# Kernel tuning notes

Measured on AMD Instinct MI355X. Metric: run time of the kernel, lower is better.

The kernel has to match this reference:

```python
import jax, jax.numpy as jnp
import numpy as np

INPUT_SIZE = 84 * 84 * 4  # 28224
FEATURE_SIZE = 1500
BATCH = 256

def setup_inputs() -> dict:
    key = jax.random.key(0)
    k_x, k_we, k_wd = jax.random.split(key, 3)
    scale_e = 1.0 / np.sqrt(INPUT_SIZE)
    scale_d = 1.0 / np.sqrt(FEATURE_SIZE)
    return {
        "x": jax.random.normal(k_x, (BATCH, INPUT_SIZE), dtype=jnp.float32),
        "W_enc": jax.random.normal(k_we, (FEATURE_SIZE, INPUT_SIZE), dtype=jnp.float32) * scale_e,
        "b_enc": jnp.zeros((FEATURE_SIZE,), dtype=jnp.float32),
        "W_dec": jax.random.normal(k_wd, (INPUT_SIZE, FEATURE_SIZE), dtype=jnp.float32) * scale_d,
        "b_dec": jnp.zeros((INPUT_SIZE,), dtype=jnp.float32),
    }

def reference(x, W_enc, b_enc, W_dec, b_dec):
    # Encoder: y_enc = sigmoid(x @ W_enc^T + b_enc), shape [B, F]
    y_enc = jax.nn.sigmoid(jnp.einsum('bi,fi->bf', x, W_enc) + b_enc)
    # Contractive (Jacobian Frobenius norm) term, closed form:
    # d y_enc[b,i] / d x[b,:] = y*(1-y) * W_enc[i,:]
    # jac_reg = sum_{b,i} (y*(1-y))^2 * ||W_enc[i,:]||^2
    s2 = jnp.square(y_enc * (1.0 - y_enc))          # [B, F]
    row_norm2 = jnp.sum(jnp.square(W_enc), axis=1)  # [F]
    jac_reg = jnp.sum(s2 * row_norm2)               # scalar
    # Decoder
    y_out = jax.nn.sigmoid(jnp.einsum('bf,if->bi', y_enc, W_dec) + b_dec)
    return y_out, jac_reg
```

## Files before the change

### kernel.cpp

```cpp
#include <hip/hip_runtime.h>
#include <hip/hip_bf16.h>


#define BATCH 256
#define IN    28224
#define FEAT  1500

typedef __attribute__((ext_vector_type(8))) short short8;
typedef __attribute__((ext_vector_type(4))) float f32x4;

__device__ __forceinline__ unsigned short f2bf(float f) {
    unsigned int u = __float_as_uint(f);
    u = (u + 0x7FFFu + ((u >> 16) & 1u)) >> 16;
    return (unsigned short)u;
}

#define ENC_KCH 1344

__global__ __launch_bounds__(256) void enc_gemm(const float* __restrict__ x,
                                                const float* __restrict__ We,
                                                float* __restrict__ preact,
                                                float* __restrict__ rn2) {
    const int n0 = blockIdx.x * 64;
    const int kbase = blockIdx.y * ENC_KCH;

    __shared__ unsigned short As[256 * 40];
    __shared__ unsigned short Bs[64 * 40];
    __shared__ float rowsq[64];

    const int t    = threadIdx.x;
    const int lane = t & 63;
    const int w    = t >> 6;
    const int l15  = lane & 15;
    const int quad = lane >> 4;

    if (t < 64) rowsq[t] = 0.0f;
    __syncthreads();

    f32x4 acc[4][4];
#pragma unroll
    for (int mt = 0; mt < 4; ++mt)
#pragma unroll
        for (int nt = 0; nt < 4; ++nt) { f32x4 z = {0.f, 0.f, 0.f, 0.f}; acc[mt][nt] = z; }

    for (int kt = 0; kt < ENC_KCH / 32; ++kt) {
        const int k0 = kbase + kt * 32;
#pragma unroll
        for (int j = 0; j < 8; ++j) {
            int idx = t + 256 * j;
            int row = idx >> 3;
            int c4  = idx & 7;
            const float4 v = *(const float4*)(x + row * IN + k0 + c4 * 4);
            ushort4 h;
            h.x = f2bf(v.x); h.y = f2bf(v.y); h.z = f2bf(v.z); h.w = f2bf(v.w);
            *(ushort4*)&As[row * 40 + c4 * 4] = h;
        }
#pragma unroll
        for (int j = 0; j < 2; ++j) {
            int idx = t + 256 * j;
            int row = idx >> 3;
            int c4  = idx & 7;
            int f   = n0 + row;
            float4 v = make_float4(0.f, 0.f, 0.f, 0.f);
            if (f < FEAT) v = *(const float4*)(We + (long)f * IN + k0 + c4 * 4);
            ushort4 h;
            h.x = f2bf(v.x); h.y = f2bf(v.y); h.z = f2bf(v.z); h.w = f2bf(v.w);
            *(ushort4*)&Bs[row * 40 + c4 * 4] = h;
            float sq = v.x * v.x + v.y * v.y + v.z * v.z + v.w * v.w;
            atomicAdd(&rowsq[row], sq);
        }
        __syncthreads();

        short8 a[4], b[4];
#pragma unroll
        for (int mt = 0; mt < 4; ++mt)
            a[mt] = *(const short8*)&As[(w * 64 + mt * 16 + l15) * 40 + quad * 8];
#pragma unroll
        for (int nt = 0; nt < 4; ++nt)
            b[nt] = *(const short8*)&Bs[(nt * 16 + l15) * 40 + quad * 8];
#pragma unroll
        for (int mt = 0; mt < 4; ++mt)
#pragma unroll
            for (int nt = 0; nt < 4; ++nt)
                acc[mt][nt] = __builtin_amdgcn_mfma_f32_16x16x32_bf16(a[mt], b[nt], acc[mt][nt], 0, 0, 0);
        __syncthreads();
    }

#pragma unroll
    for (int mt = 0; mt < 4; ++mt) {
#pragma unroll
        for (int nt = 0; nt < 4; ++nt) {
            int col = n0 + nt * 16 + l15;
            if (col < FEAT) {
#pragma unroll
                for (int r = 0; r < 4; ++r) {
                    int row = w * 64 + mt * 16 + quad * 4 + r;
                    atomicAdd(&preact[row * FEAT + col], acc[mt][nt][r]);
                }
            }
        }
    }

    if (t < 64) {
        int f = n0 + t;
        if (f < FEAT) atomicAdd(&rn2[f], rowsq[t]);
    }
}

__global__ __launch_bounds__(256) void act_jac(const float* __restrict__ preact,
                                               const float* __restrict__ be,
                                               const float* __restrict__ rn2,
                                               unsigned short* __restrict__ yenc,
                                               float* __restrict__ jac) {
    const int b = blockIdx.y;
    const int f = blockIdx.x * 256 + threadIdx.x;
    float local = 0.0f;
    unsigned short h = 0;
    if (f < FEAT) {
        float p = preact[b * FEAT + f] + be[f];
        float y = 1.0f / (1.0f + __expf(-p));
        h = f2bf(y);
        float s = y * (1.0f - y);
        local = s * s * rn2[f];
    }
    yenc[b * 1536 + f] = h;

    float v = local;
#pragma unroll
    for (int off = 32; off > 0; off >>= 1) v += __shfl_down(v, off);
    __shared__ float red[4];
    const int lane = threadIdx.x & 63;
    const int w = threadIdx.x >> 6;
    if (lane == 0) red[w] = v;
    __syncthreads();
    if (threadIdx.x == 0) atomicAdd(jac, red[0] + red[1] + red[2] + red[3]);
}

__global__ __launch_bounds__(256) void dec_gemm(const unsigned short* __restrict__ yenc,
                                                const float* __restrict__ Wd,
                                                const float* __restrict__ bd,
                                                float* __restrict__ out) {
    const int n0 = blockIdx.x * 64;

    __shared__ unsigned short As[256 * 40];
    __shared__ unsigned short Bs[64 * 40];

    const int t    = threadIdx.x;
    const int lane = t & 63;
    const int w    = t >> 6;
    const int l15  = lane & 15;
    const int quad = lane >> 4;

    f32x4 acc[4][4];
#pragma unroll
    for (int mt = 0; mt < 4; ++mt)
#pragma unroll
        for (int nt = 0; nt < 4; ++nt) { f32x4 z = {0.f, 0.f, 0.f, 0.f}; acc[mt][nt] = z; }

    for (int kt = 0; kt < 48; ++kt) {
        const int k0 = kt * 32;
#pragma unroll
        for (int j = 0; j < 4; ++j) {
            int idx = t + 256 * j;
            int row = idx >> 2;
            int c   = idx & 3;
            const short8 v = *(const short8*)(yenc + row * 1536 + k0 + c * 8);
            *(short8*)&As[row * 40 + c * 8] = v;
        }
#pragma unroll
        for (int j = 0; j < 2; ++j) {
            int idx = t + 256 * j;
            int row = idx >> 3;
            int c4  = idx & 7;
            int i   = n0 + row;
            int k   = k0 + c4 * 4;
            float4 v = make_float4(0.f, 0.f, 0.f, 0.f);
            if (k < 1500) v = *(const float4*)(Wd + (long)i * FEAT + k);
            ushort4 h;
            h.x = f2bf(v.x); h.y = f2bf(v.y); h.z = f2bf(v.z); h.w = f2bf(v.w);
            *(ushort4*)&Bs[row * 40 + c4 * 4] = h;
        }
        __syncthreads();

        short8 a[4], b[4];
#pragma unroll
        for (int mt = 0; mt < 4; ++mt)
            a[mt] = *(const short8*)&As[(w * 64 + mt * 16 + l15) * 40 + quad * 8];
#pragma unroll
        for (int nt = 0; nt < 4; ++nt)
            b[nt] = *(const short8*)&Bs[(nt * 16 + l15) * 40 + quad * 8];
#pragma unroll
        for (int mt = 0; mt < 4; ++mt)
#pragma unroll
            for (int nt = 0; nt < 4; ++nt)
                acc[mt][nt] = __builtin_amdgcn_mfma_f32_16x16x32_bf16(a[mt], b[nt], acc[mt][nt], 0, 0, 0);
        __syncthreads();
    }

#pragma unroll
    for (int mt = 0; mt < 4; ++mt) {
#pragma unroll
        for (int nt = 0; nt < 4; ++nt) {
            int col = n0 + nt * 16 + l15;
            float bias = bd[col];
#pragma unroll
            for (int r = 0; r < 4; ++r) {
                int row = w * 64 + mt * 16 + quad * 4 + r;
                float v = acc[mt][nt][r] + bias;
                out[row * IN + col] = 1.0f / (1.0f + __expf(-v));
            }
        }
    }
}

extern "C" void kernel_launch(void* const* d_in, const int* in_sizes, int n_in,
                              void* d_out, int out_size, void* d_ws, size_t ws_size,
                              hipStream_t stream) {
    const float* x  = (const float*)d_in[0];
    const float* We = (const float*)d_in[1];
    const float* be = (const float*)d_in[2];
    const float* Wd = (const float*)d_in[3];
    const float* bd = (const float*)d_in[4];
    float* out = (float*)d_out;

    char* ws = (char*)d_ws;
    float* preact          = (float*)ws;
    float* rn2             = (float*)(ws + 1536000);
    unsigned short* yenc   = (unsigned short*)(ws + 1544192);

    hipMemsetAsync(ws, 0, 1544192, stream);
    hipMemsetAsync(out + 7225344, 0, 4, stream);

    enc_gemm<<<dim3(24, 21), 256, 0, stream>>>(x, We, preact, rn2);
    act_jac<<<dim3(6, 256), 256, 0, stream>>>(preact, be, rn2, yenc, out + 7225344);
    dec_gemm<<<dim3(441, 1), 256, 0, stream>>>(yenc, Wd, bd, out);
}
```

Measured before the change: 576.1 us.

## Pre-convert x to bf16 and load MFMA operands directly from global memory

A separate kernel converts x to bf16 once into workspace. Both GEMMs then drop LDS staging and barriers, with each lane loading its MFMA fragments straight from global memory and converting weights using a cheaper perm-based bf16 pack. The encoder split-K is doubled to 42 chunks, and row norms are accumulated in registers with shuffles instead of shared-memory atomics. Costs include an extra pass over x, more preact atomics, round-half-up instead of round-to-even conversion, and strided uncoalesced global loads with no cross-wave reuse through LDS.

```diff
diff --git a/kernel.cpp b/kernel.cpp
--- a/kernel.cpp
+++ b/kernel.cpp
@@ -5,105 +5,112 @@
 #define BATCH 256
 #define IN    28224
 #define FEAT  1500
+#define FPAD  1536
 
 typedef __attribute__((ext_vector_type(8))) short short8;
 typedef __attribute__((ext_vector_type(4))) float f32x4;
 
-__device__ __forceinline__ unsigned short f2bf(float f) {
-    unsigned int u = __float_as_uint(f);
-    u = (u + 0x7FFFu + ((u >> 16) & 1u)) >> 16;
-    return (unsigned short)u;
-}
-
-#define ENC_KCH 1344
-
-__global__ __launch_bounds__(256) void enc_gemm(const float* __restrict__ x,
+__device__ __forceinline__ unsigned pack2(float lo, float hi) {
+    unsigned a = __float_as_uint(lo) + 0x8000u;
+    unsigned b = __float_as_uint(hi) + 0x8000u;
+    return __builtin_amdgcn_perm(b, a, 0x07060302);
+}
+
+__device__ __forceinline__ short8 cvt8(const float4 v0, const float4 v1) {
+    union { short8 s; unsigned u[4]; } r;
+    r.u[0] = pack2(v0.x, v0.y);
+    r.u[1] = pack2(v0.z, v0.w);
+    r.u[2] = pack2(v1.x, v1.y);
+    r.u[3] = pack2(v1.z, v1.w);
+    return r.s;
+}
+
+__global__ __launch_bounds__(256) void cvt_x(const float* __restrict__ x,
+                                             unsigned short* __restrict__ xbf) {
+    int idx = blockIdx.x * 256 + threadIdx.x;
+    float4 v = ((const float4*)x)[idx];
+    ((uint2*)xbf)[idx] = make_uint2(pack2(v.x, v.y), pack2(v.z, v.w));
+}
+
+__global__ __launch_bounds__(256) void enc_gemm(const unsigned short* __restrict__ xbf,
                                                 const float* __restrict__ We,
                                                 float* __restrict__ preact,
                                                 float* __restrict__ rn2) {
-    const int n0 = blockIdx.x * 64;
-    const int kbase = blockIdx.y * ENC_KCH;
-
-    __shared__ unsigned short As[256 * 40];
-    __shared__ unsigned short Bs[64 * 40];
-    __shared__ float rowsq[64];
-
+    const int n0   = blockIdx.x * 64;
+    const int kb   = blockIdx.y * 672;
     const int t    = threadIdx.x;
     const int lane = t & 63;
     const int w    = t >> 6;
     const int l15  = lane & 15;
     const int quad = lane >> 4;
-
-    if (t < 64) rowsq[t] = 0.0f;
-    __syncthreads();
+    const int m0   = w * 64;
+
+    const unsigned short* ap[4];
+#pragma unroll
+    for (int mt = 0; mt < 4; ++mt)
+        ap[mt] = xbf + (long)(m0 + mt * 16 + l15) * IN + quad * 8 + kb;
+
+    const float* bp[4];
+    int fcol[4];
+#pragma unroll
+    for (int nt = 0; nt < 4; ++nt) {
+        int f = n0 + nt * 16 + l15;
+        fcol[nt] = f;
+        int fc = f < FEAT ? f : FEAT - 1;
+        bp[nt] = We + (long)fc * IN + quad * 8 + kb;
+    }
 
     f32x4 acc[4][4];
 #pragma unroll
     for (int mt = 0; mt < 4; ++mt)
 #pragma unroll
         for (int nt = 0; nt < 4; ++nt) { f32x4 z = {0.f, 0.f, 0.f, 0.f}; acc[mt][nt] = z; }
-
-    for (int kt = 0; kt < ENC_KCH / 32; ++kt) {
-        const int k0 = kbase + kt * 32;
-#pragma unroll
-        for (int j = 0; j < 8; ++j) {
-            int idx = t + 256 * j;
-            int row = idx >> 3;
-            int c4  = idx & 7;
-            const float4 v = *(const float4*)(x + row * IN + k0 + c4 * 4);
-            ushort4 h;
-            h.x = f2bf(v.x); h.y = f2bf(v.y); h.z = f2bf(v.z); h.w = f2bf(v.w);
-            *(ushort4*)&As[row * 40 + c4 * 4] = h;
-        }
-#pragma unroll
-        for (int j = 0; j < 2; ++j) {
-            int idx = t + 256 * j;
-            int row = idx >> 3;
-            int c4  = idx & 7;
-            int f   = n0 + row;
-            float4 v = make_float4(0.f, 0.f, 0.f, 0.f);
-            if (f < FEAT) v = *(const float4*)(We + (long)f * IN + k0 + c4 * 4);
-            ushort4 h;
-            h.x = f2bf(v.x); h.y = f2bf(v.y); h.z = f2bf(v.z); h.w = f2bf(v.w);
-            *(ushort4*)&Bs[row * 40 + c4 * 4] = h;
-            float sq = v.x * v.x + v.y * v.y + v.z * v.z + v.w * v.w;
-            atomicAdd(&rowsq[row], sq);
-        }
-        __syncthreads();
-
-        short8 a[4], b[4];
-#pragma unroll
-        for (int mt = 0; mt < 4; ++mt)
-            a[mt] = *(const short8*)&As[(w * 64 + mt * 16 + l15) * 40 + quad * 8];
-#pragma unroll
-        for (int nt = 0; nt < 4; ++nt)
-            b[nt] = *(const short8*)&Bs[(nt * 16 + l15) * 40 + quad * 8];
+    float rsq[4] = {0.f, 0.f, 0.f, 0.f};
+
+    for (int k = 0; k < 672; k += 32) {
+        short8 a[4];
+#pragma unroll
+        for (int mt = 0; mt < 4; ++mt)
+            a[mt] = *(const short8*)(ap[mt] + k);
+        short8 bb[4];
+#pragma unroll
+        for (int nt = 0; nt < 4; ++nt) {
+            const float4 b0 = *(const float4*)(bp[nt] + k);
+            const float4 b1 = *(const float4*)(bp[nt] + k + 4);
+            bb[nt] = cvt8(b0, b1);
+            if (w == 0) {
+                rsq[nt] += b0.x * b0.x + b0.y * b0.y + b0.z * b0.z + b0.w * b0.w
+                         + b1.x * b1.x + b1.y * b1.y + b1.z * b1.z + b1.w * b1.w;
+            }
+        }
 #pragma unroll
         for (int mt = 0; mt < 4; ++mt)
 #pragma unroll
             for (int nt = 0; nt < 4; ++nt)
-                acc[mt][nt] = __builtin_amdgcn_mfma_f32_16x16x32_bf16(a[mt], b[nt], acc[mt][nt], 0, 0, 0);
-        __syncthreads();
-    }
-
-#pragma unroll
-    for (int mt = 0; mt < 4; ++mt) {
-#pragma unroll
-        for (int nt = 0; nt < 4; ++nt) {
-            int col = n0 + nt * 16 + l15;
-            if (col < FEAT) {
-#pragma unroll
-                for (int r = 0; r < 4; ++r) {
-                    int row = w * 64 + mt * 16 + quad * 4 + r;
-                    atomicAdd(&preact[row * FEAT + col], acc[mt][nt][r]);
-                }
+                acc[mt][nt] = __builtin_amdgcn_mfma_f32_16x16x32_bf16(a[mt], bb[nt], acc[mt][nt], 0, 0, 0);
+    }
+
+#pragma unroll
+    for (int nt = 0; nt < 4; ++nt) {
+        const int col = fcol[nt];
+        if (col < FEAT) {
+#pragma unroll
+            for (int mt = 0; mt < 4; ++mt) {
+                float* p = preact + (long)(m0 + mt * 16 + quad * 4) * FEAT + col;
+#pragma unroll
+                for (int r = 0; r < 4; ++r) atomicAdd(p + (long)r * FEAT, acc[mt][nt][r]);
             }
         }
     }
 
-    if (t < 64) {
-        int f = n0 + t;
-        if (f < FEAT) atomicAdd(&rn2[f], rowsq[t]);
+    if (w == 0) {
+#pragma unroll
+        for (int nt = 0; nt < 4; ++nt) {
+            float v = rsq[nt];
+            v += __shfl_xor(v, 16);
+            v += __shfl_xor(v, 32);
+            if (quad == 0 && fcol[nt] < FEAT) atomicAdd(&rn2[fcol[nt]], v);
+        }
     }
 }
 
@@ -119,19 +126,18 @@
     if (f < FEAT) {
         float p = preact[b * FEAT + f] + be[f];
         float y = 1.0f / (1.0f + __expf(-p));
-        h = f2bf(y);
+        unsigned u = __float_as_uint(y);
+        h = (unsigned short)((u + 0x7FFFu + ((u >> 16) & 1u)) >> 16);
         float s = y * (1.0f - y);
         local = s * s * rn2[f];
     }
-    yenc[b * 1536 + f] = h;
+    yenc[b * FPAD + f] = h;
 
     float v = local;
 #pragma unroll
     for (int off = 32; off > 0; off >>= 1) v += __shfl_down(v, off);
     __shared__ float red[4];
-    const int lane = threadIdx.x & 63;
-    const int w = threadIdx.x >> 6;
-    if (lane == 0) red[w] = v;
+    if ((threadIdx.x & 63) == 0) red[threadIdx.x >> 6] = v;
     __syncthreads();
     if (threadIdx.x == 0) atomicAdd(jac, red[0] + red[1] + red[2] + red[3]);
 }
@@ -140,16 +146,22 @@
                                                 const float* __restrict__ Wd,
                                                 const float* __restrict__ bd,
                                                 float* __restrict__ out) {
-    const int n0 = blockIdx.x * 64;
-
-    __shared__ unsigned short As[256 * 40];
-    __shared__ unsigned short Bs[64 * 40];
-
+    const int n0   = blockIdx.x * 64;
     const int t    = threadIdx.x;
     const int lane = t & 63;
     const int w    = t >> 6;
     const int l15  = lane & 15;
     const int quad = lane >> 4;
+    const int m0   = w * 64;
+
+    const unsigned short* ap[4];
+#pragma unroll
+    for (int mt = 0; mt < 4; ++mt)
+        ap[mt] = yenc + (long)(m0 + mt * 16 + l15) * FPAD + quad * 8;
+    const float* bp[4];
+#pragma unroll
+    for (int nt = 0; nt < 4; ++nt)
+        bp[nt] = Wd + (long)(n0 + nt * 16 + l15) * FEAT + quad * 8;
 
     f32x4 acc[4][4];
 #pragma unroll
@@ -157,57 +169,56 @@
 #pragma unroll
         for (int nt = 0; nt < 4; ++nt) { f32x4 z = {0.f, 0.f, 0.f, 0.f}; acc[mt][nt] = z; }
 
-    for (int kt = 0; kt < 48; ++kt) {
-        const int k0 = kt * 32;
-#pragma unroll
-        for (int j = 0; j < 4; ++j) {
-            int idx = t + 256 * j;
-            int row = idx >> 2;
-            int c   = idx & 3;
-            const short8 v = *(const short8*)(yenc + row * 1536 + k0 + c * 8);
-            *(short8*)&As[row * 40 + c * 8] = v;
-        }
-#pragma unroll
-        for (int j = 0; j < 2; ++j) {
-            int idx = t + 256 * j;
-            int row = idx >> 3;
-            int c4  = idx & 7;
-            int i   = n0 + row;
-            int k   = k0 + c4 * 4;
-            float4 v = make_float4(0.f, 0.f, 0.f, 0.f);
-            if (k < 1500) v = *(const float4*)(Wd + (long)i * FEAT + k);
-            ushort4 h;
-            h.x = f2bf(v.x); h.y = f2bf(v.y); h.z = f2bf(v.z); h.w = f2bf(v.w);
-            *(ushort4*)&Bs[row * 40 + c4 * 4] = h;
-        }
-        __syncthreads();
-
-        short8 a[4], b[4];
-#pragma unroll
-        for (int mt = 0; mt < 4; ++mt)
-            a[mt] = *(const short8*)&As[(w * 64 + mt * 16 + l15) * 40 + quad * 8];
-#pragma unroll
-        for (int nt = 0; nt < 4; ++nt)
-            b[nt] = *(const short8*)&Bs[(nt * 16 + l15) * 40 + quad * 8];
+    for (int k = 0; k < 1472; k += 32) {
+        short8 a[4];
+#pragma unroll
+        for (int mt = 0; mt < 4; ++mt)
+            a[mt] = *(const short8*)(ap[mt] + k);
+        short8 bb[4];
+#pragma unroll
+        for (int nt = 0; nt < 4; ++nt) {
+            const float4 b0 = *(const float4*)(bp[nt] + k);
+            const float4 b1 = *(const float4*)(bp[nt] + k + 4);
+            bb[nt] = cvt8(b0, b1);
+        }
 #pragma unroll
         for (int mt = 0; mt < 4; ++mt)
 #pragma unroll
             for (int nt = 0; nt < 4; ++nt)
-                acc[mt][nt] = __builtin_amdgcn_mfma_f32_16x16x32_bf16(a[mt], b[nt], acc[mt][nt], 0, 0, 0);
-        __syncthreads();
-    }
-
-#pragma unroll
-    for (int mt = 0; mt < 4; ++mt) {
-#pragma unroll
-        for (int nt = 0; nt < 4; ++nt) {
-            int col = n0 + nt * 16 + l15;
-            float bias = bd[col];
+                acc[mt][nt] = __builtin_amdgcn_mfma_f32_16x16x32_bf16(a[mt], bb[nt], acc[mt][nt], 0, 0, 0);
+    }
+    {
+        const float* lim = Wd + (long)IN * FEAT - 4;
+        short8 a[4];
+#pragma unroll
+        for (int mt = 0; mt < 4; ++mt)
+            a[mt] = *(const short8*)(ap[mt] + 1472);
+        short8 bb[4];
+#pragma unroll
+        for (int nt = 0; nt < 4; ++nt) {
+            const float* p0 = bp[nt] + 1472;
+            const float* p1 = p0 + 4;
+            if (p1 > lim) p1 = lim;
+            bb[nt] = cvt8(*(const float4*)p0, *(const float4*)p1);
+        }
+#pragma unroll
+        for (int mt = 0; mt < 4; ++mt)
+#pragma unroll
+            for (int nt = 0; nt < 4; ++nt)
+                acc[mt][nt] = __builtin_amdgcn_mfma_f32_16x16x32_bf16(a[mt], bb[nt], acc[mt][nt], 0, 0, 0);
+    }
+
+#pragma unroll
+    for (int nt = 0; nt < 4; ++nt) {
+        const int col = n0 + nt * 16 + l15;
+        const float bias = bd[col];
+#pragma unroll
+        for (int mt = 0; mt < 4; ++mt) {
+            const int row = m0 + mt * 16 + quad * 4;
 #pragma unroll
             for (int r = 0; r < 4; ++r) {
-                int row = w * 64 + mt * 16 + quad * 4 + r;
                 float v = acc[mt][nt][r] + bias;
-                out[row * IN + col] = 1.0f / (1.0f + __expf(-v));
+                out[(long)(row + r) * IN + col] = 1.0f / (1.0f + __expf(-v));
             }
         }
     }
@@ -224,14 +235,16 @@
     float* out = (float*)d_out;
 
     char* ws = (char*)d_ws;
-    float* preact          = (float*)ws;
-    float* rn2             = (float*)(ws + 1536000);
-    unsigned short* yenc   = (unsigned short*)(ws + 1544192);
+    float* preact        = (float*)ws;
+    float* rn2           = (float*)(ws + 1536000);
+    unsigned short* yenc = (unsigned short*)(ws + 1544192);
+    unsigned short* xbf  = (unsigned short*)(ws + 2330624);
 
     hipMemsetAsync(ws, 0, 1544192, stream);
     hipMemsetAsync(out + 7225344, 0, 4, stream);
 
-    enc_gemm<<<dim3(24, 21), 256, 0, stream>>>(x, We, preact, rn2);
+    cvt_x<<<7056, 256, 0, stream>>>(x, xbf);
+    enc_gemm<<<dim3(24, 42), 256, 0, stream>>>(xbf, We, preact, rn2);
     act_jac<<<dim3(6, 256), 256, 0, stream>>>(preact, be, rn2, yenc, out + 7225344);
-    dec_gemm<<<dim3(441, 1), 256, 0, stream>>>(yenc, Wd, bd, out);
-}
+    dec_gemm<<<441, 256, 0, stream>>>(yenc, Wd, bd, out);
+}
```

Result: slower. 616.6 us (+7.0%).
